# Kernel tuning notes

Measured on AMD Instinct MI355X. Metric: run time of the kernel, lower is better.

The kernel has to match this reference:

```python
import jax, jax.numpy as jnp
import numpy as np

B, S, D, H, E, K, V, FF, P = 1, 2048, 1024, 16, 8, 2, 32000, 4096, 4096
HD = D // H
EPS = 1e-5


def setup_inputs() -> dict:
    key = jax.random.key(0)
    ks = iter(jax.random.split(key, 64))
    w = lambda shape: jax.random.normal(next(ks), shape, jnp.float32) * 0.02
    d = {}
    d['input_ids'] = jax.random.randint(next(ks), (B, S), 0, V)
    d['embed_w'] = w((V, D))
    d['pos_w'] = w((P, D))
    for i in (0, 1):
        d[f'b{i}_ln1_g'] = jnp.ones(D); d[f'b{i}_ln1_b'] = jnp.zeros(D)
        d[f'b{i}_in_w'] = w((3 * D, D)); d[f'b{i}_in_b'] = jnp.zeros(3 * D)
        d[f'b{i}_out_w'] = w((D, D)); d[f'b{i}_out_b'] = jnp.zeros(D)
        d[f'b{i}_ln2_g'] = jnp.ones(D); d[f'b{i}_ln2_b'] = jnp.zeros(D)
    d['b0_ffn_w1'] = w((FF, D)); d['b0_ffn_b1'] = jnp.zeros(FF)
    d['b0_ffn_w2'] = w((D, FF)); d['b0_ffn_b2'] = jnp.zeros(D)
    d['b1_gate_w'] = w((E, D)); d['b1_gate_b'] = jnp.zeros(E)
    d['b1_moe_w1'] = w((E, FF, D)); d['b1_moe_b1'] = jnp.zeros((E, FF))
    d['b1_moe_w2'] = w((E, D, FF)); d['b1_moe_b2'] = jnp.zeros((E, D))
    d['norm_g'] = jnp.ones(D); d['norm_b'] = jnp.zeros(D)
    d['head_w'] = w((V, D))
    return d


def _ln(x, g, b):
    m = jnp.mean(x, -1, keepdims=True)
    v = jnp.mean(jnp.square(x - m), -1, keepdims=True)
    return (x - m) * jax.lax.rsqrt(v + EPS) * g + b


def _mha(x, in_w, in_b, out_w, out_b):
    # torch nn.MultiheadAttention (batch_first, eval mode -> no dropout)
    qkv = x @ in_w.T + in_b  # [B,S,3D]
    q, k, v = jnp.split(qkv, 3, axis=-1)
    q = q.reshape(B, S, H, HD); k = k.reshape(B, S, H, HD); v = v.reshape(B, S, H, HD)
    scores = jnp.einsum('bqhd,bkhd->bhqk', q, k) / jnp.sqrt(jnp.float32(HD))
    attn = jax.nn.softmax(scores, axis=-1)
    o = jnp.einsum('bhqk,bkhd->bqhd', attn, v).reshape(B, S, D)
    return o @ out_w.T + out_b


def _moe(h, gate_w, gate_b, w1, b1, w2, b2):
    scores = h @ gate_w.T + gate_b                       # [B,S,E]
    top_s, top_i = jax.lax.top_k(scores, K)              # [B,S,K]
    weights = jax.nn.softmax(top_s, axis=-1)             # softmax over top-k
    onehot = jax.nn.one_hot(top_i, E, dtype=h.dtype)     # [B,S,K,E]
    combine = jnp.sum(onehot * weights[..., None], axis=-2)  # [B,S,E]
    hid = jax.nn.gelu(jnp.einsum('bsd,efd->bsef', h, w1) + b1, approximate=False)
    eo = jnp.einsum('bsef,edf->bsed', hid, w2) + b2      # [B,S,E,D]
    return jnp.einsum('bsed,bse->bsd', eo, combine)


def reference(input_ids, embed_w, pos_w,
              b0_ln1_g, b0_ln1_b, b0_in_w, b0_in_b, b0_out_w, b0_out_b, b0_ln2_g, b0_ln2_b,
              b0_ffn_w1, b0_ffn_b1, b0_ffn_w2, b0_ffn_b2,
              b1_ln1_g, b1_ln1_b, b1_in_w, b1_in_b, b1_out_w, b1_out_b, b1_ln2_g, b1_ln2_b,
              b1_gate_w, b1_gate_b, b1_moe_w1, b1_moe_b1, b1_moe_w2, b1_moe_b2,
              norm_g, norm_b, head_w):
    pos = jnp.arange(S)[None, :]
    x = jnp.take(embed_w, input_ids, axis=0) + jnp.take(pos_w, pos, axis=0)
    # block 0: dense FFN
    x = x + _mha(_ln(x, b0_ln1_g, b0_ln1_b), b0_in_w, b0_in_b, b0_out_w, b0_out_b)
    h = _ln(x, b0_ln2_g, b0_ln2_b)
    ffn = jax.nn.gelu(h @ b0_ffn_w1.T + b0_ffn_b1, approximate=False) @ b0_ffn_w2.T + b0_ffn_b2
    x = x + ffn  # integration layer assumed residual add
    # block 1: MoE
    x = x + _mha(_ln(x, b1_ln1_g, b1_ln1_b), b1_in_w, b1_in_b, b1_out_w, b1_out_b)
    h = _ln(x, b1_ln2_g, b1_ln2_b)
    x = x + _moe(h, b1_gate_w, b1_gate_b, b1_moe_w1, b1_moe_b1, b1_moe_w2, b1_moe_b2)
    x = _ln(x, norm_g, norm_b)
    return x @ head_w.T
```

## Files before the change

kernel.cpp:

```cpp
#include <hip/hip_runtime.h>
#include <hip/hip_bf16.h>
#include <math.h>

typedef unsigned short ushort_t;
typedef __attribute__((ext_vector_type(8))) __bf16 bf16x8;
typedef __attribute__((ext_vector_type(4))) float f32x4;
typedef __attribute__((ext_vector_type(8))) short s8v;
typedef __attribute__((ext_vector_type(4))) short s4v;

#define SQ 2048
#define DM 1024
#define NH 16
#define HDIM 64
#define FFD 4096
#define NVOC 32000

__device__ inline float b2f(unsigned short u) {
  union { unsigned int i; float f; } x; x.i = ((unsigned int)u) << 16; return x.f;
}
__device__ inline unsigned short f2b(float f) {
  __hip_bfloat16 h = __float2bfloat16(f);
  return *reinterpret_cast<unsigned short*>(&h);
}
__device__ inline void split2(float x, ushort_t& h, ushort_t& l) {
  h = f2b(x);
  l = f2b(x - b2f(h));
}
__device__ inline float geluf(float v) {
  return 0.5f * v * (1.0f + erff(v * 0.70710678118654752f));
}
__device__ __forceinline__ void gld16(const void* g, void* l) {
  __builtin_amdgcn_global_load_lds(
      (const __attribute__((address_space(1))) void*)g,
      (__attribute__((address_space(3))) void*)l, 16, 0, 0);
}
#define MFMA __builtin_amdgcn_mfma_f32_16x16x32_bf16

template<int EPI, int NT, int KS>
__device__ __forceinline__ void gemmsp_body(
    const ushort_t* __restrict__ AH, const ushort_t* __restrict__ AL,
    int lda, long long bA,
    const ushort_t* __restrict__ BH, const ushort_t* __restrict__ BL,
    int ldb, long long bB,
    float* __restrict__ C, ushort_t* __restrict__ CH, ushort_t* __restrict__ CL,
    int ldc, long long bC, long long pC,
    int M, int N, int K, const float* __restrict__ bias, float alpha)
{
  int z = blockIdx.z, h = z / KS, kc = z % KS;
  const ushort_t* AHp = AH + (long long)h * bA + (long long)kc * K;
  const ushort_t* ALp = AL + (long long)h * bA + (long long)kc * K;
  const ushort_t* BHp = BH + (long long)h * bB + (long long)kc * K;
  const ushort_t* BLp = BL + (long long)h * bB + (long long)kc * K;
  int m0 = blockIdx.x * 128, n0 = blockIdx.y * NT;
  const int NF = NT / 32;

  __shared__ __align__(16) ushort_t sAH[128 * 32], sAL[128 * 32];
  __shared__ __align__(16) ushort_t sBH[NT * 32],  sBL[NT * 32];

  int tid = threadIdx.x, lane = tid & 63, wave = tid >> 6;
  int wr = (wave >> 1) * 64, wc = (wave & 1) * (NT >> 1);
  int l15 = lane & 15, l4 = lane >> 4;

  f32x4 acc[4][NF];
#pragma unroll
  for (int m = 0; m < 4; ++m)
#pragma unroll
    for (int n = 0; n < NF; ++n) acc[m][n] = (f32x4){0.f, 0.f, 0.f, 0.f};

  for (int k0 = 0; k0 < K; k0 += 32) {
#pragma unroll
    for (int i = 0; i < 2; ++i) {
      int fi = i * 2048 + tid * 8;
      int r = fi >> 5, chk = (fi >> 3) & 3;
      int scol = ((chk ^ ((r >> 1) & 3)) << 3);
      int ra = m0 + r; if (ra > M - 1) ra = M - 1;
      long long go = (long long)ra * lda + k0 + scol;
      gld16(AHp + go, &sAH[fi]);
      gld16(ALp + go, &sAL[fi]);
    }
#pragma unroll
    for (int i = 0; i < NT / 64; ++i) {
      int fi = i * 2048 + tid * 8;
      int r = fi >> 5, chk = (fi >> 3) & 3;
      int scol = ((chk ^ ((r >> 1) & 3)) << 3);
      int rb = n0 + r; if (rb > N - 1) rb = N - 1;
      long long go = (long long)rb * ldb + k0 + scol;
      gld16(BHp + go, &sBH[fi]);
      gld16(BLp + go, &sBL[fi]);
    }
    __syncthreads();
    bf16x8 ah[4], al[4], bh[NF], bl[NF];
#pragma unroll
    for (int m = 0; m < 4; ++m) {
      int r = wr + m * 16 + l15;
      int o = r * 32 + ((l4 ^ ((r >> 1) & 3)) << 3);
      ah[m] = *(const bf16x8*)&sAH[o];
      al[m] = *(const bf16x8*)&sAL[o];
    }
#pragma unroll
    for (int n = 0; n < NF; ++n) {
      int r = wc + n * 16 + l15;
      int o = r * 32 + ((l4 ^ ((r >> 1) & 3)) << 3);
      bh[n] = *(const bf16x8*)&sBH[o];
      bl[n] = *(const bf16x8*)&sBL[o];
    }
#pragma unroll
    for (int m = 0; m < 4; ++m)
#pragma unroll
      for (int n = 0; n < NF; ++n) {
        acc[m][n] = MFMA(ah[m], bh[n], acc[m][n], 0, 0, 0);
        acc[m][n] = MFMA(al[m], bh[n], acc[m][n], 0, 0, 0);
        acc[m][n] = MFMA(ah[m], bl[n], acc[m][n], 0, 0, 0);
      }
    __syncthreads();
  }

#pragma unroll
  for (int m = 0; m < 4; ++m) {
#pragma unroll
    for (int n = 0; n < NF; ++n) {
      int c = n0 + wc + n * 16 + l15;
      if (c >= N) continue;
      float bv = (EPI == 0 || EPI == 3 || EPI == 4) ? bias[c] : 0.f;
#pragma unroll
      for (int q = 0; q < 4; ++q) {
        int rr = m0 + wr + m * 16 + l4 * 4 + q;
        if (rr >= M) continue;
        float v = acc[m][n][q];
        if (EPI == 0) {
          ushort_t hh, ll; split2(v + bv, hh, ll);
          long long o = (long long)rr * ldc + c; CH[o] = hh; CL[o] = ll;
        } else if (EPI == 3) {
          C[(long long)rr * ldc + c] += v + bv;
        } else if (EPI == 4) {
          ushort_t hh, ll; split2(geluf(v + bv), hh, ll);
          long long o = (long long)rr * ldc + c; CH[o] = hh; CL[o] = ll;
        }
      }
    }
  }
}

#define SP_ARGS const ushort_t* AH, const ushort_t* AL, int lda, long long bA, \
    const ushort_t* BH, const ushort_t* BL, int ldb, long long bB, \
    float* C, ushort_t* CH, ushort_t* CL, int ldc, long long bC, long long pC, \
    int M, int N, int K, const float* bias, float alpha
#define SP_PASS AH, AL, lda, bA, BH, BL, ldb, bB, C, CH, CL, ldc, bC, pC, M, N, K, bias, alpha

__global__ __launch_bounds__(256) void k_qkv (SP_ARGS) { gemmsp_body<0,128,1>(SP_PASS); }
__global__ __launch_bounds__(256) void k_outp(SP_ARGS) { gemmsp_body<3, 64,1>(SP_PASS); }
__global__ __launch_bounds__(256) void k_ffn1(SP_ARGS) { gemmsp_body<4,128,1>(SP_PASS); }
__global__ __launch_bounds__(256) void k_ffn2(SP_ARGS) { gemmsp_body<3, 64,1>(SP_PASS); }

__global__ __launch_bounds__(256)
void k_attn(const ushort_t* __restrict__ qkvH, const ushort_t* __restrict__ qkvL,
            const ushort_t* __restrict__ VtH, const ushort_t* __restrict__ VtL,
            ushort_t* __restrict__ aH, ushort_t* __restrict__ aL)
{
  int f = blockIdx.x + blockIdx.y * gridDim.x;
  int logical = (f & 7) * 64 + (f >> 3);
  int q0 = (logical & 31) * 64;
  int h  = logical >> 5;

  __shared__ __align__(16) ushort_t sKH[4096], sKL[4096];
  __shared__ __align__(16) ushort_t sVH[4096], sVL[4096];
  __shared__ __align__(16) ushort_t sPH[4096], sPL[4096];

  int tid = threadIdx.x, lane = tid & 63, wave = tid >> 6;
  int l15 = lane & 15, l4 = lane >> 4;

  bf16x8 qh[2], ql[2];
  {
    long long base = (long long)(q0 + wave * 16 + l15) * (3 * DM) + h * 64 + l4 * 8;
    qh[0] = *(const bf16x8*)(qkvH + base);
    qh[1] = *(const bf16x8*)(qkvH + base + 32);
    ql[0] = *(const bf16x8*)(qkvL + base);
    ql[1] = *(const bf16x8*)(qkvL + base + 32);
  }

  float mrow[4], lrow[4];
  f32x4 Oacc[4];
#pragma unroll
  for (int r = 0; r < 4; ++r) { mrow[r] = -1e30f; lrow[r] = 0.f; }
#pragma unroll
  for (int n = 0; n < 4; ++n) Oacc[n] = (f32x4){0.f, 0.f, 0.f, 0.f};

  for (int kt = 0; kt < SQ / 64; ++kt) {
#pragma unroll
    for (int i = 0; i < 2; ++i) {
      int idx = i * 2048 + tid * 8;
      int row = idx >> 6, chk = (idx >> 3) & 7;
      int scol = ((chk ^ (row & 7)) << 3);
      long long gk = (long long)(kt * 64 + row) * (3 * DM) + DM + h * 64 + scol;
      long long gv = (long long)(h * 64 + row) * SQ + kt * 64 + scol;
      gld16(qkvH + gk, &sKH[idx]);
      gld16(qkvL + gk, &sKL[idx]);
      gld16(VtH + gv, &sVH[idx]);
      gld16(VtL + gv, &sVL[idx]);
    }
    __syncthreads();

    f32x4 S[4];
#pragma unroll
    for (int n = 0; n < 4; ++n) S[n] = (f32x4){0.f, 0.f, 0.f, 0.f};
#pragma unroll
    for (int kk = 0; kk < 64; kk += 32) {
      int kkI = kk >> 5;
      bf16x8 qhf = qh[kkI], qlf = ql[kkI];
#pragma unroll
      for (int n = 0; n < 4; ++n) {
        int br = n * 16 + l15;
        int bo = br * 64 + ((((kk >> 3) + l4) ^ (br & 7)) << 3);
        bf16x8 kh = *(const bf16x8*)&sKH[bo];
        bf16x8 kl = *(const bf16x8*)&sKL[bo];
        S[n] = MFMA(qhf, kh, S[n], 0, 0, 0);
        S[n] = MFMA(qlf, kh, S[n], 0, 0, 0);
        S[n] = MFMA(qhf, kl, S[n], 0, 0, 0);
      }
    }
    float tm[4], ts[4];
#pragma unroll
    for (int r = 0; r < 4; ++r) {
#pragma unroll
      for (int n = 0; n < 4; ++n) S[n][r] *= 0.125f;
      tm[r] = fmaxf(fmaxf(S[0][r], S[1][r]), fmaxf(S[2][r], S[3][r]));
    }
#pragma unroll
    for (int mk = 1; mk <= 8; mk <<= 1)
#pragma unroll
      for (int r = 0; r < 4; ++r) tm[r] = fmaxf(tm[r], __shfl_xor(tm[r], mk));
#pragma unroll
    for (int r = 0; r < 4; ++r) {
      float mn = fmaxf(mrow[r], tm[r]);
      float corr = __expf(mrow[r] - mn);
      mrow[r] = mn;
      float s = 0.f;
#pragma unroll
      for (int n = 0; n < 4; ++n) { S[n][r] = __expf(S[n][r] - mn); s += S[n][r]; }
      ts[r] = s;
      lrow[r] *= corr;
#pragma unroll
      for (int n = 0; n < 4; ++n) Oacc[n][r] *= corr;
    }
#pragma unroll
    for (int mk = 1; mk <= 8; mk <<= 1)
#pragma unroll
      for (int r = 0; r < 4; ++r) ts[r] += __shfl_xor(ts[r], mk);
#pragma unroll
    for (int r = 0; r < 4; ++r) lrow[r] += ts[r];

    {
      ushort_t* pH = &sPH[wave * 1024];
      ushort_t* pL = &sPL[wave * 1024];
#pragma unroll
      for (int n = 0; n < 4; ++n)
#pragma unroll
        for (int r = 0; r < 4; ++r) {
          int row = l4 * 4 + r, col = n * 16 + l15;
          int ad = row * 64 + (((col >> 3) ^ (row & 7)) << 3) + (col & 7);
          ushort_t hh, ll; split2(S[n][r], hh, ll);
          pH[ad] = hh; pL[ad] = ll;
        }
    }
    __syncthreads();
#pragma unroll
    for (int kk = 0; kk < 64; kk += 32) {
      int ao = wave * 1024 + l15 * 64 + ((((kk >> 3) + l4) ^ (l15 & 7)) << 3);
      bf16x8 ph = *(const bf16x8*)&sPH[ao];
      bf16x8 pl = *(const bf16x8*)&sPL[ao];
#pragma unroll
      for (int n = 0; n < 4; ++n) {
        int br = n * 16 + l15;
        int bo = br * 64 + ((((kk >> 3) + l4) ^ (br & 7)) << 3);
        bf16x8 vh = *(const bf16x8*)&sVH[bo];
        bf16x8 vl = *(const bf16x8*)&sVL[bo];
        Oacc[n] = MFMA(ph, vh, Oacc[n], 0, 0, 0);
        Oacc[n] = MFMA(pl, vh, Oacc[n], 0, 0, 0);
        Oacc[n] = MFMA(ph, vl, Oacc[n], 0, 0, 0);
      }
    }
    __syncthreads();
  }

#pragma unroll
  for (int n = 0; n < 4; ++n)
#pragma unroll
    for (int r = 0; r < 4; ++r) {
      int q = q0 + wave * 16 + l4 * 4 + r;
      int d = h * 64 + n * 16 + l15;
      float val = Oacc[n][r] / lrow[r];
      ushort_t hh, ll; split2(val, hh, ll);
      long long o = (long long)q * DM + d;
      aH[o] = hh; aL[o] = ll;
    }
}

template<int EPI, int BSRC, int SWAP, int KS, int XS>
__device__ __forceinline__ void gemm16_body(
    const ushort_t* __restrict__ A, int lda, long long bA,
    const void* __restrict__ Bv, int ldb, long long bB,
    void* __restrict__ Cv, int ldc, long long bC, long long pC,
    int M, int N, int K, const float* __restrict__ bias, int bBias,
    const int* __restrict__ offs)
{
  int bz = blockIdx.z;
  int z = bz / KS, kc = bz % KS;
  int Kc = K / KS;
  const ushort_t* Ap = A + (long long)z * bA + (long long)kc * Kc;
  int rowStart = 0, Meff = M;
  if (offs) { rowStart = offs[z]; Meff = offs[z + 1] - rowStart; }
  int bx = blockIdx.x, by = blockIdx.y;
  if (XS) {
    int flat = bx + by * gridDim.x;
    int cpx = (gridDim.x * gridDim.y) >> 3;
    int s = (flat & 7) * cpx + (flat >> 3);
    bx = s % gridDim.x; by = s / gridDim.x;
  }
  int m0 = (SWAP ? by : bx) * 128;
  if (m0 >= Meff) return;
  int n0 = (SWAP ? bx : by) * 128;

  __shared__ __align__(16) char smem[32768];
  ushort_t* As = (ushort_t*)smem;
  ushort_t* Bs = (ushort_t*)(smem + 16384);

  int tid = threadIdx.x, lane = tid & 63, wave = tid >> 6;
  int wr = (wave >> 1) * 64, wc = (wave & 1) * 64;
  int l15 = lane & 15, l4 = lane >> 4;

  f32x4 acc[4][4];
#pragma unroll
  for (int m = 0; m < 4; ++m)
#pragma unroll
    for (int n = 0; n < 4; ++n) acc[m][n] = (f32x4){0.f, 0.f, 0.f, 0.f};

  for (int k0 = 0; k0 < Kc; k0 += 64) {
#pragma unroll
    for (int i = 0; i < 4; ++i) {
      int idx = i * 2048 + tid * 8;
      int row = idx >> 6, chk = (idx >> 3) & 7;
      int scol = ((chk ^ (row & 7)) << 3);
      int ra = m0 + row; if (ra > Meff - 1) ra = Meff - 1;
      gld16(Ap + (long long)(rowStart + ra) * lda + k0 + scol, &As[idx]);
    }
    if (BSRC == 1) {
      const ushort_t* Bp = (const ushort_t*)Bv + (long long)z * bB + (long long)kc * Kc;
#pragma unroll
      for (int i = 0; i < 4; ++i) {
        int idx = i * 2048 + tid * 8;
        int row = idx >> 6, chk = (idx >> 3) & 7;
        int scol = ((chk ^ (row & 7)) << 3);
        int rb = n0 + row; if (rb > N - 1) rb = N - 1;
        gld16(Bp + (long long)rb * ldb + k0 + scol, &Bs[idx]);
      }
    } else {
      const float* Bf = (const float*)Bv + (long long)z * bB + (long long)kc * Kc;
#pragma unroll
      for (int i = 0; i < 8; ++i) {
        int g = tid + i * 256;
        int r = g >> 4, c4 = (g & 15) * 4;
        int rb = n0 + r; if (rb > N - 1) rb = N - 1;
        float4 fv = *(const float4*)(Bf + (long long)rb * ldb + k0 + c4);
        s4v o; o[0] = (short)f2b(fv.x); o[1] = (short)f2b(fv.y);
        o[2] = (short)f2b(fv.z); o[3] = (short)f2b(fv.w);
        int dst = r * 64 + (((c4 >> 3) ^ (r & 7)) << 3) + (c4 & 7);
        *(s4v*)&Bs[dst] = o;
      }
    }
    __syncthreads();
#pragma unroll
    for (int kk = 0; kk < 64; kk += 32) {
      bf16x8 af[4], bfr[4];
#pragma unroll
      for (int m = 0; m < 4; ++m) {
        int r = wr + m * 16 + l15;
        af[m] = *(const bf16x8*)&As[r * 64 + ((((kk >> 3) + l4) ^ (r & 7)) << 3)];
      }
#pragma unroll
      for (int n = 0; n < 4; ++n) {
        int r = wc + n * 16 + l15;
        bfr[n] = *(const bf16x8*)&Bs[r * 64 + ((((kk >> 3) + l4) ^ (r & 7)) << 3)];
      }
#pragma unroll
      for (int m = 0; m < 4; ++m)
#pragma unroll
        for (int n = 0; n < 4; ++n)
          acc[m][n] = MFMA(af[m], bfr[n], acc[m][n], 0, 0, 0);
    }
    __syncthreads();
  }

  if (EPI == 6 || EPI == 7) {
    float* fE = (float*)smem;
#pragma unroll
    for (int h2 = 0; h2 < 2; ++h2) {
      if ((wave >> 1) == h2) {
#pragma unroll
        for (int m = 0; m < 4; ++m)
#pragma unroll
          for (int n = 0; n < 4; ++n)
#pragma unroll
            for (int q = 0; q < 4; ++q)
              fE[(m * 16 + l4 * 4 + q) * 128 + wc + n * 16 + l15] = acc[m][n][q];
      }
      __syncthreads();
#pragma unroll
      for (int i = 0; i < 8; ++i) {
        int lin = tid + i * 256;
        int row = lin >> 5, c4 = (lin & 31) << 2;
        int gr = m0 + h2 * 64 + row;
        if (gr < Meff) {
          float4 v4 = *(const float4*)&fE[row * 128 + c4];
          long long crow = rowStart + gr;
          float* dst = (float*)Cv + (EPI == 7 ? (long long)kc * pC : 0LL)
                       + crow * ldc + n0 + c4;
          *(float4*)dst = v4;
        }
      }
      __syncthreads();
    }
    return;
  }

#pragma unroll
  for (int m = 0; m < 4; ++m) {
#pragma unroll
    for (int n = 0; n < 4; ++n) {
      int c = n0 + wc + n * 16 + l15;
      if (c >= N) continue;
      float bv = (EPI == 2) ? bias[(long long)z * bBias + c] : 0.f;
#pragma unroll
      for (int q = 0; q < 4; ++q) {
        int rr = m0 + wr + m * 16 + l4 * 4 + q;
        if (rr >= Meff) continue;
        float v = acc[m][n][q];
        long long crow = rowStart + rr;
        if (EPI == 2)
          ((ushort_t*)Cv)[crow * ldc + (long long)z * bC + c] = f2b(geluf(v + bv));
      }
    }
  }
}

#define G16_ARGS const ushort_t* A, int lda, long long bA, const void* Bv, \
    int ldb, long long bB, void* Cv, int ldc, long long bC, long long pC, \
    int M, int N, int K, const float* bias, int bBias, const int* offs
#define G16_PASS A, lda, bA, Bv, ldb, bB, Cv, ldc, bC, pC, M, N, K, bias, bBias, offs

__global__ __launch_bounds__(256) void k_moe1   (G16_ARGS) { gemm16_body<2,1,1,1,0>(G16_PASS); }
__global__ __launch_bounds__(256) void k_moe2   (G16_ARGS) { gemm16_body<7,1,1,2,0>(G16_PASS); }
__global__ __launch_bounds__(256) void k_head_bf(G16_ARGS) { gemm16_body<6,1,0,1,1>(G16_PASS); }
__global__ __launch_bounds__(256) void k_head_f (G16_ARGS) { gemm16_body<6,0,0,1,1>(G16_PASS); }

__global__ __launch_bounds__(256)
void cvt_split(const float* __restrict__ s, ushort_t* __restrict__ dh,
               ushort_t* __restrict__ dl, int n4)
{
  int i = blockIdx.x * blockDim.x + threadIdx.x;
  int stride = gridDim.x * blockDim.x;
  for (; i < n4; i += stride) {
    float4 f = ((const float4*)s)[i];
    s4v h, l; ushort_t hh, ll;
    split2(f.x, hh, ll); h[0] = (short)hh; l[0] = (short)ll;
    split2(f.y, hh, ll); h[1] = (short)hh; l[1] = (short)ll;
    split2(f.z, hh, ll); h[2] = (short)hh; l[2] = (short)ll;
    split2(f.w, hh, ll); h[3] = (short)hh; l[3] = (short)ll;
    ((s4v*)dh)[i] = h; ((s4v*)dl)[i] = l;
  }
}

__global__ __launch_bounds__(256)
void cvt_bf16(const float* __restrict__ s, ushort_t* __restrict__ d, int n4)
{
  int i = blockIdx.x * blockDim.x + threadIdx.x;
  int stride = gridDim.x * blockDim.x;
  for (; i < n4; i += stride) {
    float4 f = ((const float4*)s)[i];
    s4v o; o[0] = (short)f2b(f.x); o[1] = (short)f2b(f.y);
    o[2] = (short)f2b(f.z); o[3] = (short)f2b(f.w);
    ((s4v*)d)[i] = o;
  }
}

__global__ __launch_bounds__(256)
void embed_kernel(const int* __restrict__ ids, const float* __restrict__ ew,
                  const float* __restrict__ pw, float* __restrict__ x)
{
  int srow = blockIdx.x, tid = threadIdx.x;
  int id = ids[srow];
  const float4 e = *(const float4*)(ew + (long long)id * DM + tid * 4);
  const float4 p = *(const float4*)(pw + (long long)srow * DM + tid * 4);
  float4* xr = (float4*)(x + (long long)srow * DM) + tid;
  *xr = make_float4(e.x + p.x, e.y + p.y, e.z + p.z, e.w + p.w);
}

template<int MODE>
__global__ __launch_bounds__(256)
void ln_kernel(const float* __restrict__ x, const float* __restrict__ g,
               const float* __restrict__ b, ushort_t* __restrict__ outH,
               ushort_t* __restrict__ outL)
{
  int row = blockIdx.x, tid = threadIdx.x;
  float4 v = ((const float4*)(x + (long long)row * DM))[tid];
  __shared__ float sm1[4], sm2[4];
  float s = v.x + v.y + v.z + v.w;
  for (int o = 32; o > 0; o >>= 1) s += __shfl_down(s, o);
  if ((tid & 63) == 0) sm1[tid >> 6] = s;
  __syncthreads();
  float mean = (sm1[0] + sm1[1] + sm1[2] + sm1[3]) * (1.0f / DM);
  float d0 = v.x - mean, d1 = v.y - mean, d2 = v.z - mean, d3 = v.w - mean;
  float q = d0 * d0 + d1 * d1 + d2 * d2 + d3 * d3;
  for (int o = 32; o > 0; o >>= 1) q += __shfl_down(q, o);
  if ((tid & 63) == 0) sm2[tid >> 6] = q;
  __syncthreads();
  float var = (sm2[0] + sm2[1] + sm2[2] + sm2[3]) * (1.0f / DM);
  float rstd = rsqrtf(var + 1e-5f);
  float4 gv = ((const float4*)g)[tid];
  float4 bv = ((const float4*)b)[tid];
  float o0 = d0 * rstd * gv.x + bv.x, o1 = d1 * rstd * gv.y + bv.y;
  float o2 = d2 * rstd * gv.z + bv.z, o3 = d3 * rstd * gv.w + bv.w;
  long long base = (long long)row * DM + tid * 4;
  if (MODE == 0) {
    ushort_t hh, ll;
    split2(o0, hh, ll); outH[base + 0] = hh; outL[base + 0] = ll;
    split2(o1, hh, ll); outH[base + 1] = hh; outL[base + 1] = ll;
    split2(o2, hh, ll); outH[base + 2] = hh; outL[base + 2] = ll;
    split2(o3, hh, ll); outH[base + 3] = hh; outL[base + 3] = ll;
  } else {
    outH[base + 0] = f2b(o0); outH[base + 1] = f2b(o1);
    outH[base + 2] = f2b(o2); outH[base + 3] = f2b(o3);
  }
}

__global__ __launch_bounds__(256)
void transpose_v2(const ushort_t* __restrict__ qH, const ushort_t* __restrict__ qL,
                  ushort_t* __restrict__ vH, ushort_t* __restrict__ vL)
{
  __shared__ ushort_t tH[64][65], tL[64][65];
  int j0 = blockIdx.x * 64, h = blockIdx.y;
  int tid = threadIdx.x;
  int jr = tid >> 2, d0 = (tid & 3) * 16;
  long long so = (long long)(j0 + jr) * (3 * DM) + 2 * DM + h * 64 + d0;
#pragma unroll
  for (int i = 0; i < 16; ++i) { tH[jr][d0 + i] = qH[so + i]; tL[jr][d0 + i] = qL[so + i]; }
  __syncthreads();
  int dd = tid >> 2, jc = (tid & 3) * 16;
  long long dofs = (long long)(h * 64 + dd) * SQ + j0 + jc;
#pragma unroll
  for (int i = 0; i < 16; ++i) { vH[dofs + i] = tH[jc + i][dd]; vL[dofs + i] = tL[jc + i][dd]; }
}

__global__ __launch_bounds__(256)
void ln_gate_top2(const float* __restrict__ x, const float* __restrict__ g,
                  const float* __restrict__ b, const float* __restrict__ gw,
                  const float* __restrict__ gb, int* __restrict__ topi,
                  float* __restrict__ topw, int* __restrict__ counts,
                  ushort_t* __restrict__ outH)
{
  int row = blockIdx.x, tid = threadIdx.x;
  float4 v = ((const float4*)(x + (long long)row * DM))[tid];
  __shared__ float sm1[4], sm2[4];
  __shared__ float se[8][4];
  float s = v.x + v.y + v.z + v.w;
  for (int o = 32; o > 0; o >>= 1) s += __shfl_down(s, o);
  if ((tid & 63) == 0) sm1[tid >> 6] = s;
  __syncthreads();
  float mean = (sm1[0] + sm1[1] + sm1[2] + sm1[3]) * (1.0f / DM);
  float d0 = v.x - mean, d1 = v.y - mean, d2 = v.z - mean, d3 = v.w - mean;
  float q = d0 * d0 + d1 * d1 + d2 * d2 + d3 * d3;
  for (int o = 32; o > 0; o >>= 1) q += __shfl_down(q, o);
  if ((tid & 63) == 0) sm2[tid >> 6] = q;
  __syncthreads();
  float var = (sm2[0] + sm2[1] + sm2[2] + sm2[3]) * (1.0f / DM);
  float rstd = rsqrtf(var + 1e-5f);
  float4 gv = ((const float4*)g)[tid];
  float4 bv = ((const float4*)b)[tid];
  float h0 = d0 * rstd * gv.x + bv.x, h1 = d1 * rstd * gv.y + bv.y;
  float h2 = d2 * rstd * gv.z + bv.z, h3 = d3 * rstd * gv.w + bv.w;
  long long base = (long long)row * DM + tid * 4;
  outH[base + 0] = f2b(h0); outH[base + 1] = f2b(h1);
  outH[base + 2] = f2b(h2); outH[base + 3] = f2b(h3);
#pragma unroll
  for (int e = 0; e < 8; ++e) {
    float4 w = ((const float4*)(gw + (long long)e * DM))[tid];
    float p = h0 * w.x + h1 * w.y + h2 * w.z + h3 * w.w;
    for (int o = 32; o > 0; o >>= 1) p += __shfl_down(p, o);
    if ((tid & 63) == 0) se[e][tid >> 6] = p;
  }
  __syncthreads();
  if (tid == 0) {
    float sc[8];
#pragma unroll
    for (int e = 0; e < 8; ++e)
      sc[e] = se[e][0] + se[e][1] + se[e][2] + se[e][3] + gb[e];
    int i1 = 0; float m1 = sc[0];
    for (int e = 1; e < 8; ++e) if (sc[e] > m1) { m1 = sc[e]; i1 = e; }
    int i2 = -1; float m2 = -1e30f;
    for (int e = 0; e < 8; ++e) if (e != i1 && sc[e] > m2) { m2 = sc[e]; i2 = e; }
    float e2 = __expf(m2 - m1);
    float w1 = 1.f / (1.f + e2);
    topi[row * 2] = i1; topi[row * 2 + 1] = i2;
    topw[row * 2] = w1; topw[row * 2 + 1] = 1.f - w1;
    atomicAdd(&counts[i1], 1);
    atomicAdd(&counts[i2], 1);
  }
}

__global__ void moe_zero(int* counts) { if (threadIdx.x < 8) counts[threadIdx.x] = 0; }

__global__ void moe_prefix(const int* __restrict__ counts, int* __restrict__ offs,
                           int* __restrict__ cursors)
{
  if (threadIdx.x == 0 && blockIdx.x == 0) {
    int a = 0;
    for (int e = 0; e < 8; ++e) { offs[e] = a; a += counts[e]; cursors[e] = 0; }
    offs[8] = a;
  }
}

__global__ __launch_bounds__(256)
void moe_gather(const ushort_t* __restrict__ hH, const int* __restrict__ topi,
                const float* __restrict__ topw, const int* __restrict__ offs,
                int* __restrict__ cursors, int* __restrict__ tokIdx,
                float* __restrict__ tokW, int* __restrict__ slotOf,
                ushort_t* __restrict__ Xg)
{
  int tok = blockIdx.x, tid = threadIdx.x;
  __shared__ int s0s, s1s;
  if (tid == 0) {
    int e0 = topi[tok * 2], e1 = topi[tok * 2 + 1];
    int s0 = offs[e0] + atomicAdd(&cursors[e0], 1);
    int s1 = offs[e1] + atomicAdd(&cursors[e1], 1);
    tokIdx[s0] = tok; tokW[s0] = topw[tok * 2];
    tokIdx[s1] = tok; tokW[s1] = topw[tok * 2 + 1];
    slotOf[tok * 2] = s0; slotOf[tok * 2 + 1] = s1;
    s0s = s0; s1s = s1;
  }
  __syncthreads();
  s4v v = ((const s4v*)(hH + (long long)tok * DM))[tid];
  ((s4v*)(Xg + (long long)s0s * DM))[tid] = v;
  ((s4v*)(Xg + (long long)s1s * DM))[tid] = v;
}

__global__ __launch_bounds__(256)
void moe_reduce(float* __restrict__ x, const float* __restrict__ eo, long long pC,
                const int* __restrict__ slotOf, const int* __restrict__ topi,
                const float* __restrict__ topw, const float* __restrict__ b2)
{
  int tok = blockIdx.x, tid = threadIdx.x;
  int s0 = slotOf[tok * 2], s1 = slotOf[tok * 2 + 1];
  int e0 = topi[tok * 2], e1 = topi[tok * 2 + 1];
  float w0 = topw[tok * 2], w1 = topw[tok * 2 + 1];
  float4 a  = ((const float4*)(eo + (long long)s0 * DM))[tid];
  float4 a2 = ((const float4*)(eo + pC + (long long)s0 * DM))[tid];
  float4 b  = ((const float4*)(eo + (long long)s1 * DM))[tid];
  float4 b2v= ((const float4*)(eo + pC + (long long)s1 * DM))[tid];
  float4 ba = ((const float4*)(b2 + (long long)e0 * DM))[tid];
  float4 bb = ((const float4*)(b2 + (long long)e1 * DM))[tid];
  float4* xr = (float4*)(x + (long long)tok * DM) + tid;
  float4 xv = *xr;
  xv.x += w0 * (a.x + a2.x + ba.x) + w1 * (b.x + b2v.x + bb.x);
  xv.y += w0 * (a.y + a2.y + ba.y) + w1 * (b.y + b2v.y + bb.y);
  xv.z += w0 * (a.z + a2.z + ba.z) + w1 * (b.z + b2v.z + bb.z);
  xv.w += w0 * (a.w + a2.w + ba.w) + w1 * (b.w + b2v.w + bb.w);
  *xr = xv;
}

extern "C" void kernel_launch(void* const* d_in, const int* in_sizes, int n_in,
                              void* d_out, int out_size, void* d_ws, size_t ws_size,
                              hipStream_t stream)
{
  const int* ids = (const int*)d_in[0];
  const float* embed_w = (const float*)d_in[1];
  const float* pos_w   = (const float*)d_in[2];
  const float* ln1_g[2] = {(const float*)d_in[3],  (const float*)d_in[11]};
  const float* ln1_b[2] = {(const float*)d_in[4],  (const float*)d_in[12]};
  const float* in_w[2]  = {(const float*)d_in[5],  (const float*)d_in[13]};
  const float* in_b[2]  = {(const float*)d_in[6],  (const float*)d_in[14]};
  const float* out_w[2] = {(const float*)d_in[7],  (const float*)d_in[15]};
  const float* out_b[2] = {(const float*)d_in[8],  (const float*)d_in[16]};
  const float* ln2_g[2] = {(const float*)d_in[9],  (const float*)d_in[17]};
  const float* ln2_b[2] = {(const float*)d_in[10], (const float*)d_in[18]};
  const float* ffn_w1 = (const float*)d_in[19];
  const float* ffn_b1 = (const float*)d_in[20];
  const float* ffn_w2 = (const float*)d_in[21];
  const float* ffn_b2 = (const float*)d_in[22];
  const float* gate_w = (const float*)d_in[23];
  const float* gate_b = (const float*)d_in[24];
  const float* moe_w1 = (const float*)d_in[25];
  const float* moe_b1 = (const float*)d_in[26];
  const float* moe_w2 = (const float*)d_in[27];
  const float* moe_b2 = (const float*)d_in[28];
  const float* norm_g = (const float*)d_in[29];
  const float* norm_b = (const float*)d_in[30];
  const float* head_w = (const float*)d_in[31];

  char* ob = (char*)d_out;
  size_t off = 0;
  auto alloc = [&](size_t bytes) {
    char* p = ob + off;
    off = (off + bytes + 255) & ~(size_t)255;
    return p;
  };
  float*    x      = (float*)alloc((size_t)SQ * DM * 4);
  ushort_t* hbufH  = (ushort_t*)alloc((size_t)SQ * DM * 2);
  ushort_t* hbufL  = (ushort_t*)alloc((size_t)SQ * DM * 2);
  ushort_t* qkvH   = (ushort_t*)alloc((size_t)SQ * 3 * DM * 2);
  ushort_t* qkvL   = (ushort_t*)alloc((size_t)SQ * 3 * DM * 2);
  ushort_t* VtH    = (ushort_t*)alloc((size_t)NH * HDIM * SQ * 2);
  ushort_t* VtL    = (ushort_t*)alloc((size_t)NH * HDIM * SQ * 2);
  char*     resv   = (char*)alloc((size_t)32 << 20);
  ushort_t* attnH  = (ushort_t*)alloc((size_t)SQ * DM * 2);
  ushort_t* attnL  = (ushort_t*)alloc((size_t)SQ * DM * 2);
  ushort_t* Xg     = (ushort_t*)alloc((size_t)2 * SQ * DM * 2);
  int*      topi   = (int*)alloc(SQ * 2 * 4);
  float*    topw   = (float*)alloc(SQ * 2 * 4);
  int*      tokIdx = (int*)alloc(2 * SQ * 4);
  float*    tokW   = (float*)alloc(2 * SQ * 4);
  int*      slotOf = (int*)alloc(2 * SQ * 4);
  int*      counts = (int*)alloc(256);
  int*      offsb  = (int*)alloc(256);
  int*      cursors= (int*)alloc(256);
  ushort_t* ffnH   = (ushort_t*)alloc((size_t)SQ * FFD * 2);
  ushort_t* ffnL   = (ushort_t*)alloc((size_t)SQ * FFD * 2);
  float*    eo     = (float*)alloc((size_t)2 * 2 * SQ * DM * 4);
  ushort_t* inwH[2], *inwL[2], *outwH[2], *outwL[2];
  ushort_t* wsplit0 = (ushort_t*)alloc(0);
  inwH[0]  = (ushort_t*)alloc((size_t)3 * DM * DM * 2);
  inwL[0]  = (ushort_t*)alloc((size_t)3 * DM * DM * 2);
  inwH[1]  = (ushort_t*)alloc((size_t)3 * DM * DM * 2);
  inwL[1]  = (ushort_t*)alloc((size_t)3 * DM * DM * 2);
  outwH[0] = (ushort_t*)alloc((size_t)DM * DM * 2);
  outwL[0] = (ushort_t*)alloc((size_t)DM * DM * 2);
  outwH[1] = (ushort_t*)alloc((size_t)DM * DM * 2);
  outwL[1] = (ushort_t*)alloc((size_t)DM * DM * 2);
  ushort_t* f1H = (ushort_t*)alloc((size_t)FFD * DM * 2);
  ushort_t* f1L = (ushort_t*)alloc((size_t)FFD * DM * 2);
  ushort_t* f2H = (ushort_t*)alloc((size_t)DM * FFD * 2);
  ushort_t* f2L = (ushort_t*)alloc((size_t)DM * FFD * 2);
  ushort_t* moe_w1b = wsplit0;
  ushort_t* moe_w2b = qkvH;
  ushort_t* moehid  = ffnH;
  const long long eoPC = (long long)2 * SQ * DM;
  ushort_t* hfin    = (ushort_t*)d_ws;
  bool wsBig = ws_size >= ((size_t)70 << 20);
  ushort_t* head_wb = (ushort_t*)((char*)d_ws + ((size_t)4 << 20));
  (void)resv;

  moe_zero<<<1, 64, 0, stream>>>(counts);
  embed_kernel<<<SQ, 256, 0, stream>>>(ids, embed_w, pos_w, x);
  cvt_split<<<512, 256, 0, stream>>>(in_w[0], inwH[0], inwL[0], 3 * DM * DM / 4);
  cvt_split<<<512, 256, 0, stream>>>(in_w[1], inwH[1], inwL[1], 3 * DM * DM / 4);
  cvt_split<<<512, 256, 0, stream>>>(out_w[0], outwH[0], outwL[0], DM * DM / 4);
  cvt_split<<<512, 256, 0, stream>>>(out_w[1], outwH[1], outwL[1], DM * DM / 4);
  cvt_split<<<512, 256, 0, stream>>>(ffn_w1, f1H, f1L, FFD * DM / 4);
  cvt_split<<<512, 256, 0, stream>>>(ffn_w2, f2H, f2L, DM * FFD / 4);
  if (wsBig)
    cvt_bf16<<<1024, 256, 0, stream>>>(head_w, head_wb, NVOC * DM / 4);

  for (int L = 0; L < 2; ++L) {
    ln_kernel<0><<<SQ, 256, 0, stream>>>(x, ln1_g[L], ln1_b[L], hbufH, hbufL);
    k_qkv<<<dim3(16, 24, 1), 256, 0, stream>>>(
        hbufH, hbufL, DM, 0, inwH[L], inwL[L], DM, 0,
        nullptr, qkvH, qkvL, 3 * DM, 0, 0,
        SQ, 3 * DM, DM, in_b[L], 1.f);
    transpose_v2<<<dim3(SQ / 64, NH), 256, 0, stream>>>(qkvH, qkvL, VtH, VtL);
    k_attn<<<dim3(SQ / 64, NH), 256, 0, stream>>>(qkvH, qkvL, VtH, VtL,
                                                  attnH, attnL);
    k_outp<<<dim3(16, 16, 1), 256, 0, stream>>>(
        attnH, attnL, DM, 0, outwH[L], outwL[L], DM, 0,
        x, nullptr, nullptr, DM, 0, 0,
        SQ, DM, DM, out_b[L], 1.f);
    if (L == 0) {
      ln_kernel<0><<<SQ, 256, 0, stream>>>(x, ln2_g[0], ln2_b[0], hbufH, hbufL);
      k_ffn1<<<dim3(16, 32, 1), 256, 0, stream>>>(
          hbufH, hbufL, DM, 0, f1H, f1L, DM, 0,
          nullptr, ffnH, ffnL, FFD, 0, 0,
          SQ, FFD, DM, ffn_b1, 1.f);
      k_ffn2<<<dim3(16, 16, 1), 256, 0, stream>>>(
          ffnH, ffnL, FFD, 0, f2H, f2L, FFD, 0,
          x, nullptr, nullptr, DM, 0, 0,
          SQ, DM, FFD, ffn_b2, 1.f);
    } else {
      cvt_bf16<<<2048, 256, 0, stream>>>(moe_w1, moe_w1b, 8 * FFD * DM / 4);
      cvt_bf16<<<2048, 256, 0, stream>>>(moe_w2, moe_w2b, 8 * DM * FFD / 4);
      ln_gate_top2<<<SQ, 256, 0, stream>>>(x, ln2_g[1], ln2_b[1], gate_w, gate_b,
                                           topi, topw, counts, hbufH);
      moe_prefix<<<1, 64, 0, stream>>>(counts, offsb, cursors);
      moe_gather<<<SQ, 256, 0, stream>>>(hbufH, topi, topw, offsb, cursors,
                                         tokIdx, tokW, slotOf, Xg);
      k_moe1<<<dim3(32, 16, 8), 256, 0, stream>>>(
          Xg, DM, 0, moe_w1b, DM, (long long)FFD * DM,
          moehid, FFD, 0, 0, SQ, FFD, DM, moe_b1, FFD, offsb);
      k_moe2<<<dim3(8, 16, 16), 256, 0, stream>>>(
          moehid, FFD, 0, moe_w2b, FFD, (long long)DM * FFD,
          eo, DM, 0, eoPC, SQ, DM, FFD, nullptr, 0, offsb);
      moe_reduce<<<SQ, 256, 0, stream>>>(x, eo, eoPC, slotOf, topi, topw, moe_b2);
    }
  }
  ln_kernel<1><<<SQ, 256, 0, stream>>>(x, norm_g, norm_b, hfin, nullptr);
  if (wsBig)
    k_head_bf<<<dim3(16, 250, 1), 256, 0, stream>>>(
        hfin, DM, 0, head_wb, DM, 0, d_out, NVOC, 0, 0,
        SQ, NVOC, DM, nullptr, 0, nullptr);
  else
    k_head_f<<<dim3(16, 250, 1), 256, 0, stream>>>(
        hfin, DM, 0, head_w, DM, 0, d_out, NVOC, 0, 0,
        SQ, NVOC, DM, nullptr, 0, nullptr);
}
```

Before: 1.332 ms.

## Split-K the out-projection and FFN2 GEMMs with a separate reduce-add kernel

The out-projection and FFN2 GEMMs, which launched only 256 blocks, now split K across 4 and 2 z-slices. Each slice writes fp32 partials to a scratch buffer, and a new reduce_add kernel adds the bias and accumulates the partials into the residual. The change also fuses pairs of weight-conversion launches into one 2D-grid kernel, folds the MoE counter zeroing into the embed kernel, and uses nontemporal stores for the head logits. Together these aim to raise GPU occupancy and cut launch overhead, at the cost of extra partial-buffer traffic and one more kernel per GEMM.

```diff
diff --git a/kernel.cpp b/kernel.cpp
--- a/kernel.cpp
+++ b/kernel.cpp
@@ -130,6 +130,8 @@
         if (EPI == 0) {
           ushort_t hh, ll; split2(v + bv, hh, ll);
           long long o = (long long)rr * ldc + c; CH[o] = hh; CL[o] = ll;
+        } else if (EPI == 2) {
+          C[(long long)kc * pC + (long long)rr * ldc + (long long)h * bC + c] = v;
         } else if (EPI == 3) {
           C[(long long)rr * ldc + c] += v + bv;
         } else if (EPI == 4) {
@@ -148,9 +150,28 @@
 #define SP_PASS AH, AL, lda, bA, BH, BL, ldb, bB, C, CH, CL, ldc, bC, pC, M, N, K, bias, alpha
 
 __global__ __launch_bounds__(256) void k_qkv (SP_ARGS) { gemmsp_body<0,128,1>(SP_PASS); }
-__global__ __launch_bounds__(256) void k_outp(SP_ARGS) { gemmsp_body<3, 64,1>(SP_PASS); }
+__global__ __launch_bounds__(256) void k_outp(SP_ARGS) { gemmsp_body<2, 64,4>(SP_PASS); }
 __global__ __launch_bounds__(256) void k_ffn1(SP_ARGS) { gemmsp_body<4,128,1>(SP_PASS); }
-__global__ __launch_bounds__(256) void k_ffn2(SP_ARGS) { gemmsp_body<3, 64,1>(SP_PASS); }
+__global__ __launch_bounds__(256) void k_ffn2(SP_ARGS) { gemmsp_body<2, 64,2>(SP_PASS); }
+
+template<int NP>
+__global__ __launch_bounds__(256)
+void reduce_add(float* __restrict__ x, const float* __restrict__ P, long long pC,
+                const float* __restrict__ bias)
+{
+  int row = blockIdx.x, tid = threadIdx.x;
+  long long o = (long long)row * DM + tid * 4;
+  float4 xv = *(float4*)(x + o);
+  float4 bv = *(const float4*)(bias + tid * 4);
+  float sx = bv.x, sy = bv.y, sz = bv.z, sw = bv.w;
+#pragma unroll
+  for (int p = 0; p < NP; ++p) {
+    float4 v = *(const float4*)(P + (long long)p * pC + o);
+    sx += v.x; sy += v.y; sz += v.z; sw += v.w;
+  }
+  xv.x += sx; xv.y += sy; xv.z += sz; xv.w += sw;
+  *(float4*)(x + o) = xv;
+}
 
 __global__ __launch_bounds__(256)
 void k_attn(const ushort_t* __restrict__ qkvH, const ushort_t* __restrict__ qkvL,
@@ -410,11 +431,12 @@
         int row = lin >> 5, c4 = (lin & 31) << 2;
         int gr = m0 + h2 * 64 + row;
         if (gr < Meff) {
-          float4 v4 = *(const float4*)&fE[row * 128 + c4];
+          f32x4 v4 = *(const f32x4*)&fE[row * 128 + c4];
           long long crow = rowStart + gr;
           float* dst = (float*)Cv + (EPI == 7 ? (long long)kc * pC : 0LL)
                        + crow * ldc + n0 + c4;
-          *(float4*)dst = v4;
+          if (EPI == 6) __builtin_nontemporal_store(v4, (f32x4*)dst);
+          else          *(f32x4*)dst = v4;
         }
       }
       __syncthreads();
@@ -453,9 +475,14 @@
 __global__ __launch_bounds__(256) void k_head_f (G16_ARGS) { gemm16_body<6,0,0,1,1>(G16_PASS); }
 
 __global__ __launch_bounds__(256)
-void cvt_split(const float* __restrict__ s, ushort_t* __restrict__ dh,
-               ushort_t* __restrict__ dl, int n4)
-{
+void cvt_split2(const float* __restrict__ s0, ushort_t* __restrict__ dh0,
+                ushort_t* __restrict__ dl0,
+                const float* __restrict__ s1, ushort_t* __restrict__ dh1,
+                ushort_t* __restrict__ dl1, int n4)
+{
+  const float* s = blockIdx.y ? s1 : s0;
+  ushort_t* dh = blockIdx.y ? dh1 : dh0;
+  ushort_t* dl = blockIdx.y ? dl1 : dl0;
   int i = blockIdx.x * blockDim.x + threadIdx.x;
   int stride = gridDim.x * blockDim.x;
   for (; i < n4; i += stride) {
@@ -484,9 +511,11 @@
 
 __global__ __launch_bounds__(256)
 void embed_kernel(const int* __restrict__ ids, const float* __restrict__ ew,
-                  const float* __restrict__ pw, float* __restrict__ x)
+                  const float* __restrict__ pw, float* __restrict__ x,
+                  int* __restrict__ counts)
 {
   int srow = blockIdx.x, tid = threadIdx.x;
+  if (srow == 0 && tid < 8) counts[tid] = 0;
   int id = ids[srow];
   const float4 e = *(const float4*)(ew + (long long)id * DM + tid * 4);
   const float4 p = *(const float4*)(pw + (long long)srow * DM + tid * 4);
@@ -605,8 +634,6 @@
     atomicAdd(&counts[i2], 1);
   }
 }
-
-__global__ void moe_zero(int* counts) { if (threadIdx.x < 8) counts[threadIdx.x] = 0; }
 
 __global__ void moe_prefix(const int* __restrict__ counts, int* __restrict__ offs,
                            int* __restrict__ cursors)
@@ -741,20 +768,21 @@
   ushort_t* moe_w1b = wsplit0;
   ushort_t* moe_w2b = qkvH;
   ushort_t* moehid  = ffnH;
+  float*    pp      = eo;
   const long long eoPC = (long long)2 * SQ * DM;
+  const long long ppPC = (long long)SQ * DM;
   ushort_t* hfin    = (ushort_t*)d_ws;
   bool wsBig = ws_size >= ((size_t)70 << 20);
   ushort_t* head_wb = (ushort_t*)((char*)d_ws + ((size_t)4 << 20));
   (void)resv;
 
-  moe_zero<<<1, 64, 0, stream>>>(counts);
-  embed_kernel<<<SQ, 256, 0, stream>>>(ids, embed_w, pos_w, x);
-  cvt_split<<<512, 256, 0, stream>>>(in_w[0], inwH[0], inwL[0], 3 * DM * DM / 4);
-  cvt_split<<<512, 256, 0, stream>>>(in_w[1], inwH[1], inwL[1], 3 * DM * DM / 4);
-  cvt_split<<<512, 256, 0, stream>>>(out_w[0], outwH[0], outwL[0], DM * DM / 4);
-  cvt_split<<<512, 256, 0, stream>>>(out_w[1], outwH[1], outwL[1], DM * DM / 4);
-  cvt_split<<<512, 256, 0, stream>>>(ffn_w1, f1H, f1L, FFD * DM / 4);
-  cvt_split<<<512, 256, 0, stream>>>(ffn_w2, f2H, f2L, DM * FFD / 4);
+  embed_kernel<<<SQ, 256, 0, stream>>>(ids, embed_w, pos_w, x, counts);
+  cvt_split2<<<dim3(512, 2), 256, 0, stream>>>(
+      in_w[0], inwH[0], inwL[0], in_w[1], inwH[1], inwL[1], 3 * DM * DM / 4);
+  cvt_split2<<<dim3(512, 2), 256, 0, stream>>>(
+      out_w[0], outwH[0], outwL[0], out_w[1], outwH[1], outwL[1], DM * DM / 4);
+  cvt_split2<<<dim3(512, 2), 256, 0, stream>>>(
+      ffn_w1, f1H, f1L, ffn_w2, f2H, f2L, FFD * DM / 4);
   if (wsBig)
     cvt_bf16<<<1024, 256, 0, stream>>>(head_w, head_wb, NVOC * DM / 4);
 
@@ -767,20 +795,22 @@
     transpose_v2<<<dim3(SQ / 64, NH), 256, 0, stream>>>(qkvH, qkvL, VtH, VtL);
     k_attn<<<dim3(SQ / 64, NH), 256, 0, stream>>>(qkvH, qkvL, VtH, VtL,
                                                   attnH, attnL);
-    k_outp<<<dim3(16, 16, 1), 256, 0, stream>>>(
+    k_outp<<<dim3(16, 16, 4), 256, 0, stream>>>(
         attnH, attnL, DM, 0, outwH[L], outwL[L], DM, 0,
-        x, nullptr, nullptr, DM, 0, 0,
-        SQ, DM, DM, out_b[L], 1.f);
+        pp, nullptr, nullptr, DM, 0, ppPC,
+        SQ, DM, DM / 4, nullptr, 1.f);
+    reduce_add<4><<<SQ, 256, 0, stream>>>(x, pp, ppPC, out_b[L]);
     if (L == 0) {
       ln_kernel<0><<<SQ, 256, 0, stream>>>(x, ln2_g[0], ln2_b[0], hbufH, hbufL);
       k_ffn1<<<dim3(16, 32, 1), 256, 0, stream>>>(
           hbufH, hbufL, DM, 0, f1H, f1L, DM, 0,
           nullptr, ffnH, ffnL, FFD, 0, 0,
           SQ, FFD, DM, ffn_b1, 1.f);
-      k_ffn2<<<dim3(16, 16, 1), 256, 0, stream>>>(
+      k_ffn2<<<dim3(16, 16, 2), 256, 0, stream>>>(
           ffnH, ffnL, FFD, 0, f2H, f2L, FFD, 0,
-          x, nullptr, nullptr, DM, 0, 0,
-          SQ, DM, FFD, ffn_b2, 1.f);
+          pp, nullptr, nullptr, DM, 0, ppPC,
+          SQ, DM, FFD / 2, nullptr, 1.f);
+      reduce_add<2><<<SQ, 256, 0, stream>>>(x, pp, ppPC, ffn_b2);
     } else {
       cvt_bf16<<<2048, 256, 0, stream>>>(moe_w1, moe_w1b, 8 * FFD * DM / 4);
       cvt_bf16<<<2048, 256, 0, stream>>>(moe_w2, moe_w2b, 8 * DM * FFD / 4);
```

Measured after the change: 1.235 ms. 7.3% less time.
